# Kernel tuning notes

Hardware: AMD Instinct MI355X
Metric: run time of the kernel (lower is better)

The kernel has to match this reference:

```python
import jax, jax.numpy as jnp
import numpy as np

B, N, DIM = 1, 2048, 2048
H, KVH = 32, 4                 # query heads, kv heads
D = DIM // H                   # head_dim = 64
REP = H // KVH                 # queries per kv = 8
KV_DIM = D * KVH               # 256


def _rope_tables(n, d, base=10000.0):
    inv = 1.0 / (base ** (np.arange(0, d, 2, dtype=np.float32) / d))
    t = np.arange(n, dtype=np.float32)
    freqs = np.outer(t, inv)                      # [n, d/2]
    emb = np.concatenate([freqs, freqs], axis=-1)  # [n, d]
    return jnp.asarray(np.cos(emb)), jnp.asarray(np.sin(emb))


def setup_inputs() -> dict:
    key = jax.random.key(0)
    ks = jax.random.split(key, 5)
    s = 0.02
    cos, sin = _rope_tables(N, D)
    return {
        "x": jax.random.normal(ks[0], (B, N, DIM), jnp.float32),
        "Wq": jax.random.normal(ks[1], (DIM, DIM), jnp.float32) * s,
        "Wk": jax.random.normal(ks[2], (KV_DIM, DIM), jnp.float32) * s,
        "Wv": jax.random.normal(ks[3], (KV_DIM, DIM), jnp.float32) * s,
        "Wo": jax.random.normal(ks[4], (DIM, DIM), jnp.float32) * s,
        "cos": cos,
        "sin": sin,
    }


def _rotate_half(t):
    d2 = t.shape[-1] // 2
    return jnp.concatenate([-t[..., d2:], t[..., :d2]], axis=-1)


def reference(x, Wq, Wk, Wv, Wo, cos, sin):
    b, n, _ = x.shape
    # projections (nn.Linear: x @ W.T)
    q = (x @ Wq.T).reshape(b, n, H, D).transpose(0, 2, 1, 3)     # b h n d
    k = (x @ Wk.T).reshape(b, n, KVH, D).transpose(0, 2, 1, 3)   # b g n d
    v = (x @ Wv.T).reshape(b, n, KVH, D).transpose(0, 2, 1, 3)
    # RoPE
    c = cos[None, None, :, :]
    s = sin[None, None, :, :]
    q = q * c + _rotate_half(q) * s
    k = k * c + _rotate_half(k) * s
    # expand KV heads (repeat_interleave over head dim)
    k = jnp.repeat(k, REP, axis=1)   # b h n d
    v = jnp.repeat(v, REP, axis=1)
    # causal attention with materialized scores (faithful to source)
    scale = 1.0 / jnp.sqrt(jnp.asarray(D, x.dtype))
    scores = jnp.einsum('bhld,bhsd->bhls', q, k) * scale
    causal = jnp.tril(jnp.ones((n, n), bool))
    scores = jnp.where(causal[None, None], scores, jnp.asarray(-jnp.inf, x.dtype))
    attn = jax.nn.softmax(scores, axis=-1)
    y = jnp.einsum('bhls,bhsd->bhld', attn, v)       # b h n d
    y = y.transpose(0, 2, 1, 3).reshape(b, n, DIM)   # b n (h d)
    return y @ Wo.T
```

## Files before the change

kernel.cpp:

```cpp
#include <hip/hip_runtime.h>

typedef unsigned short u16;
typedef __attribute__((ext_vector_type(8))) short short8;
typedef __attribute__((ext_vector_type(4))) float floatx4;

#define N_TOK 2048
#define DIM   2048
#define NH    32
#define NKVH  4
#define HD    64
#define KVD   256

__device__ __forceinline__ float bf2f(u16 u) {
  union { unsigned i; float f; } c; c.i = ((unsigned)u) << 16; return c.f;
}
__device__ __forceinline__ u16 f2bf(float f) {
  union { float f; unsigned i; } c; c.f = f;
  unsigned x = c.i;
  return (u16)((x + 0x7fffu + ((x >> 16) & 1u)) >> 16);
}

__device__ __forceinline__ void gload16(const u16* g, u16* l) {
#if defined(__has_builtin) && __has_builtin(__builtin_amdgcn_global_load_lds)
  __builtin_amdgcn_global_load_lds(
      (const __attribute__((address_space(1))) void*)g,
      (__attribute__((address_space(3))) void*)l, 16, 0, 0);
#else
  *(short8*)l = *(const short8*)g;
#endif
}

#define C_X  1048576
#define C_WQ 2097152
#define C_WK 2228224
#define C_WV 2359296
#define C_WO 3407872
__global__ __launch_bounds__(256) void cvt_all(const float* __restrict__ x,
                                               const float* __restrict__ wq,
                                               const float* __restrict__ wk,
                                               const float* __restrict__ wv,
                                               const float* __restrict__ wo,
                                               u16* __restrict__ dst) {
  int i = blockIdx.x * 256 + threadIdx.x;
  const float* src; int off;
  if      (i < C_X)  { src = x;  off = 0; }
  else if (i < C_WQ) { src = wq; off = C_X; }
  else if (i < C_WK) { src = wk; off = C_WQ; }
  else if (i < C_WV) { src = wv; off = C_WK; }
  else               { src = wo; off = C_WV; }
  float4 v = ((const float4*)src)[i - off];
  ushort4 o;
  o.x = f2bf(v.x); o.y = f2bf(v.y); o.z = f2bf(v.z); o.w = f2bf(v.w);
  ((ushort4*)dst)[i] = o;
}


__global__ __launch_bounds__(256) void gemm_qkv(const u16* __restrict__ A,
                                                const u16* __restrict__ Wq,
                                                const u16* __restrict__ Wk,
                                                const u16* __restrict__ Wv,
                                                const float* __restrict__ cs,
                                                const float* __restrict__ sn,
                                                u16* __restrict__ Qp,
                                                u16* __restrict__ Kp,
                                                u16* __restrict__ Vp) {
  __shared__ __align__(16) u16 As[2][64 * 32];
  __shared__ __align__(16) u16 Bs[2][128 * 32];
  const int tid  = threadIdx.x;
  const int lane = tid & 63;
  const int w    = tid >> 6;
  const int r    = lane & 15, q = lane >> 4;
  const int tm = blockIdx.x & 31;
  const int tn = blockIdx.x >> 5;
  const int wm = w & 1, wn = w >> 1;
  const int K = DIM;

  const u16* W; int wrow0;
  if (tn < 16)      { W = Wq; wrow0 = tn * 128; }
  else if (tn < 18) { W = Wk; wrow0 = (tn - 16) * 128; }
  else              { W = Wv; wrow0 = (tn - 18) * 128; }

  const int srow   = tid >> 2;
  const int schunk = (tid & 3) ^ ((srow >> 1) & 3);
  const int scol   = schunk * 8;
  const u16* ga = A + (size_t)(tm * 64 + srow) * K + scol;
  const u16* gb = W + (size_t)(wrow0 + srow) * K + scol;

  const int rsw = (q ^ ((r >> 1) & 3)) * 8;

  floatx4 acc[2][4];
#pragma unroll
  for (int a = 0; a < 2; ++a)
#pragma unroll
    for (int b = 0; b < 4; ++b) acc[a][b] = (floatx4){0.f, 0.f, 0.f, 0.f};

  auto stage = [&](int b, int k0) {
    gload16(ga + k0, &As[b][tid * 8]);
    gload16(gb + k0, &Bs[b][tid * 8]);
    gload16(gb + k0 + (size_t)64 * K, &Bs[b][tid * 8 + 2048]);
  };

  stage(0, 0);
  __syncthreads();
  int cb = 0;
  for (int k0 = 0; k0 < K; k0 += 32) {
    if (k0 + 32 < K) stage(cb ^ 1, k0 + 32);

    short8 af[2], bf[4];
#pragma unroll
    for (int mi = 0; mi < 2; ++mi)
      af[mi] = *(const short8*)&As[cb][(wm * 32 + mi * 16 + r) * 32 + rsw];
#pragma unroll
    for (int nj = 0; nj < 4; ++nj)
      bf[nj] = *(const short8*)&Bs[cb][(wn * 64 + nj * 16 + r) * 32 + rsw];
#pragma unroll
    for (int mi = 0; mi < 2; ++mi)
#pragma unroll
      for (int nj = 0; nj < 4; ++nj)
        acc[mi][nj] = __builtin_amdgcn_mfma_f32_16x16x32_bf16(af[mi], bf[nj], acc[mi][nj], 0, 0, 0);

    __syncthreads();
    cb ^= 1;
  }

  if (tn < 18) {
    const int head = (tn < 16) ? (tn * 2 + wn) : ((tn - 16) * 2 + wn);
#pragma unroll
    for (int mi = 0; mi < 2; ++mi)
#pragma unroll
      for (int g = 0; g < 4; ++g) {
        int row = tm * 64 + wm * 32 + mi * 16 + 4 * q + g;
        const float* crow  = cs + (size_t)row * 64;
        const float* srow2 = sn + (size_t)row * 64;
#pragma unroll
        for (int nj = 0; nj < 2; ++nj) {
          int d = nj * 16 + r;
          float x0 = acc[mi][nj][g];
          float x1 = acc[mi][nj + 2][g];
          float o0 = x0 * crow[d]      - x1 * srow2[d];
          float o1 = x1 * crow[d + 32] + x0 * srow2[d + 32];
          int qq = d >> 3, j = d & 7;
          int lslot = (qq * 16 + (row & 15)) * 8 + j;
          if (tn < 16) {
            int sq = row >> 5, ii = (row >> 4) & 1;
            size_t base = ((size_t)(head * 64 + sq) * 4 + ii * 2) * 512 + lslot;
            Qp[base]       = f2bf(o0);
            Qp[base + 512] = f2bf(o1);
          } else {
            int kt = row >> 6, t = (row >> 4) & 3;
            size_t base = ((size_t)(head * 32 + kt) * 8 + t * 2) * 512 + lslot;
            Kp[base]       = f2bf(o0);
            Kp[base + 512] = f2bf(o1);
          }
        }
      }
  } else {
#pragma unroll
    for (int mi = 0; mi < 2; ++mi)
#pragma unroll
      for (int nj = 0; nj < 4; ++nj) {
        int col  = (tn - 18) * 128 + wn * 64 + nj * 16 + r;
        int kvh  = col >> 6;
        int t    = (col & 63) >> 4;
        int rr   = col & 15;
        int row0 = tm * 64 + wm * 32 + mi * 16 + 4 * q;
        int kt   = row0 >> 6;
        int wk   = row0 & 63;
        int s    = wk >> 5;
        int qq   = (wk & 31) >> 3;
        int j0   = wk & 7;
        uint2 pk;
        pk.x = (unsigned)f2bf(acc[mi][nj][0]) | ((unsigned)f2bf(acc[mi][nj][1]) << 16);
        pk.y = (unsigned)f2bf(acc[mi][nj][2]) | ((unsigned)f2bf(acc[mi][nj][3]) << 16);
        size_t idx = ((size_t)(kvh * 32 + kt) * 8 + s * 4 + t) * 512 + (qq * 16 + rr) * 8 + j0;
        *(uint2*)(Vp + idx) = pk;
      }
  }
}

__global__ __launch_bounds__(256) void gemm_out(const u16* __restrict__ A,
                                                const u16* __restrict__ W,
                                                float* __restrict__ C) {
  __shared__ __align__(16) u16 As[2][64 * 32];
  __shared__ __align__(16) u16 Bs[2][128 * 32];
  const int tid  = threadIdx.x;
  const int lane = tid & 63;
  const int w    = tid >> 6;
  const int r    = lane & 15, q = lane >> 4;
  const int tn = blockIdx.x & 15;
  const int tm = blockIdx.x >> 4;
  const int wm = w & 1, wn = w >> 1;
  const int K = DIM;

  const int srow   = tid >> 2;
  const int schunk = (tid & 3) ^ ((srow >> 1) & 3);
  const int scol   = schunk * 8;
  const u16* ga = A + (size_t)(tm * 64 + srow) * K + scol;
  const u16* gb = W + (size_t)(tn * 128 + srow) * K + scol;

  const int rsw = (q ^ ((r >> 1) & 3)) * 8;

  floatx4 acc[2][4];
#pragma unroll
  for (int a = 0; a < 2; ++a)
#pragma unroll
    for (int b = 0; b < 4; ++b) acc[a][b] = (floatx4){0.f, 0.f, 0.f, 0.f};

  auto stage = [&](int b, int k0) {
    gload16(ga + k0, &As[b][tid * 8]);
    gload16(gb + k0, &Bs[b][tid * 8]);
    gload16(gb + k0 + (size_t)64 * K, &Bs[b][tid * 8 + 2048]);
  };

  stage(0, 0);
  __syncthreads();
  int cb = 0;
  for (int k0 = 0; k0 < K; k0 += 32) {
    if (k0 + 32 < K) stage(cb ^ 1, k0 + 32);

    short8 af[2], bf[4];
#pragma unroll
    for (int mi = 0; mi < 2; ++mi)
      af[mi] = *(const short8*)&As[cb][(wm * 32 + mi * 16 + r) * 32 + rsw];
#pragma unroll
    for (int nj = 0; nj < 4; ++nj)
      bf[nj] = *(const short8*)&Bs[cb][(wn * 64 + nj * 16 + r) * 32 + rsw];
#pragma unroll
    for (int mi = 0; mi < 2; ++mi)
#pragma unroll
      for (int nj = 0; nj < 4; ++nj)
        acc[mi][nj] = __builtin_amdgcn_mfma_f32_16x16x32_bf16(af[mi], bf[nj], acc[mi][nj], 0, 0, 0);

    __syncthreads();
    cb ^= 1;
  }

#pragma unroll
  for (int mi = 0; mi < 2; ++mi)
#pragma unroll
    for (int g = 0; g < 4; ++g) {
      int row = tm * 64 + wm * 32 + mi * 16 + 4 * q + g;
#pragma unroll
      for (int nj = 0; nj < 4; ++nj)
        C[(size_t)row * DIM + tn * 128 + wn * 64 + nj * 16 + r] = acc[mi][nj][g];
    }
}

__global__ __launch_bounds__(128, 2) void attn_mfma(const u16* __restrict__ Qp,
                                                    const u16* __restrict__ Kp,
                                                    const u16* __restrict__ Vp,
                                                    u16* __restrict__ Yb) {
  __shared__ __align__(16) u16 Pl[2][32][72];
  __shared__ float OcA[32][66];
  __shared__ float OcB[32][66];
  __shared__ float LcA[2][64], LcB[2][64];
  const int tid  = threadIdx.x;
  const int lane = tid & 63;
  const int w    = tid >> 6;
  const int r    = lane & 15;
  const int q    = lane >> 4;
  const int p    = blockIdx.x;
  const int h    = blockIdx.y;
  const int kvh  = h >> 3;
  const int jA   = 63 - p;
  const int jB   = p;
  const int baseqA = jA * 32, baseqB = jB * 32;
  const int tA = (jA >> 1) + 1, tB = (jB >> 1) + 1;
  const int ktmaxA = tA - 1, ktmaxB = tB - 1;

  short8 qfA[2][2], qfB[2][2];
#pragma unroll
  for (int i = 0; i < 2; ++i)
#pragma unroll
    for (int c = 0; c < 2; ++c) {
      qfA[i][c] = *(const short8*)(Qp + ((size_t)(h * 64 + jA) * 4 + i * 2 + c) * 512 + lane * 8);
      qfB[i][c] = *(const short8*)(Qp + ((size_t)(h * 64 + jB) * 4 + i * 2 + c) * 512 + lane * 8);
    }

  floatx4 OA[2][4], OB[2][4];
  float lsumA[2], lsumB[2];
#pragma unroll
  for (int i = 0; i < 2; ++i) {
    lsumA[i] = 0.f; lsumB[i] = 0.f;
#pragma unroll
    for (int t = 0; t < 4; ++t) {
      OA[i][t] = (floatx4){0.f, 0.f, 0.f, 0.f};
      OB[i][t] = (floatx4){0.f, 0.f, 0.f, 0.f};
    }
  }

  const u16* Kbase = Kp + (size_t)(kvh * 32) * 8 * 512;
  const u16* Vbase = Vp + (size_t)(kvh * 32) * 8 * 512;

  auto loadK = [&](int kt, short8 (&kf)[4][2]) {
    const u16* kb = Kbase + (size_t)kt * 8 * 512 + lane * 8;
#pragma unroll
    for (int t = 0; t < 4; ++t) {
      kf[t][0] = *(const short8*)(kb + (t * 2 + 0) * 512);
      kf[t][1] = *(const short8*)(kb + (t * 2 + 1) * 512);
    }
  };

  auto body = [&](int kt, int ktmax, int baseq,
                  short8 (&qf)[2][2], floatx4 (&O)[2][4], float (&lsum)[2],
                  short8 (&kc)[4][2], short8 (&kn)[4][2]) {
    short8 vb[2][4];
    {
      const u16* vbp = Vbase + (size_t)kt * 8 * 512 + lane * 8;
#pragma unroll
      for (int s = 0; s < 2; ++s)
#pragma unroll
        for (int t = 0; t < 4; ++t)
          vb[s][t] = *(const short8*)(vbp + (s * 4 + t) * 512);
    }

    loadK(kt + 2 <= ktmax ? kt + 2 : ktmax, kn);

    floatx4 ST[2][4];
#pragma unroll
    for (int i = 0; i < 2; ++i)
#pragma unroll
      for (int t = 0; t < 4; ++t) ST[i][t] = (floatx4){0.f, 0.f, 0.f, 0.f};
#pragma unroll
    for (int t = 0; t < 4; ++t)
#pragma unroll
      for (int i = 0; i < 2; ++i) {
        ST[i][t] = __builtin_amdgcn_mfma_f32_16x16x32_bf16(kc[t][0], qf[i][0], ST[i][t], 0, 0, 0);
        ST[i][t] = __builtin_amdgcn_mfma_f32_16x16x32_bf16(kc[t][1], qf[i][1], ST[i][t], 0, 0, 0);
      }

    if (kt == ktmax) {
#pragma unroll
      for (int i = 0; i < 2; ++i) {
        int qrow = baseq + 16 * i + r;
#pragma unroll
        for (int t = 0; t < 4; ++t) {
          int key = kt * 64 + 16 * t + 4 * q;
#pragma unroll
          for (int g = 0; g < 4; ++g)
            if (key + g > qrow) ST[i][t][g] = -1e30f;
        }
      }
    }

#pragma unroll
    for (int i = 0; i < 2; ++i)
#pragma unroll
      for (int t = 0; t < 4; ++t) {
        float p0 = __expf(0.125f * ST[i][t][0]);
        float p1 = __expf(0.125f * ST[i][t][1]);
        float p2 = __expf(0.125f * ST[i][t][2]);
        float p3 = __expf(0.125f * ST[i][t][3]);
        lsum[i] += (p0 + p1) + (p2 + p3);
        uint2 pk;
        pk.x = (unsigned)f2bf(p0) | ((unsigned)f2bf(p1) << 16);
        pk.y = (unsigned)f2bf(p2) | ((unsigned)f2bf(p3) << 16);
        *(uint2*)&Pl[w][16 * i + r][16 * t + 4 * q] = pk;
      }

#pragma unroll
    for (int s = 0; s < 2; ++s)
#pragma unroll
      for (int i = 0; i < 2; ++i) {
        short8 pa = *(const short8*)&Pl[w][16 * i + r][32 * s + 8 * q];
#pragma unroll
        for (int t = 0; t < 4; ++t)
          O[i][t] = __builtin_amdgcn_mfma_f32_16x16x32_bf16(pa, vb[s][t], O[i][t], 0, 0, 0);
      }
  };

  auto runloop = [&](int start, int ktmax, int baseq,
                     short8 (&qf)[2][2], floatx4 (&O)[2][4], float (&lsum)[2]) {
    if (start > ktmax) return;
    short8 kA[4][2], kB[4][2];
    loadK(start, kA);
    for (int kt = start; kt <= ktmax; kt += 4) {
      body(kt, ktmax, baseq, qf, O, lsum, kA, kB);
      if (kt + 2 <= ktmax) body(kt + 2, ktmax, baseq, qf, O, lsum, kB, kA);
    }
  };

  runloop(w, ktmaxA, baseqA, qfA, OA, lsumA);
  const int sB = (w + tA) & 1;
  runloop(sB, ktmaxB, baseqB, qfB, OB, lsumB);

  if (w == 1) {
#pragma unroll
    for (int i = 0; i < 2; ++i) {
#pragma unroll
      for (int t = 0; t < 4; ++t)
#pragma unroll
        for (int g = 0; g < 4; ++g)
          OcA[(i * 4 + t) * 4 + g][lane] = OA[i][t][g];
      LcA[i][lane] = lsumA[i];
    }
  } else {
#pragma unroll
    for (int i = 0; i < 2; ++i) {
#pragma unroll
      for (int t = 0; t < 4; ++t)
#pragma unroll
        for (int g = 0; g < 4; ++g)
          OcB[(i * 4 + t) * 4 + g][lane] = OB[i][t][g];
      LcB[i][lane] = lsumB[i];
    }
  }
  __syncthreads();

  auto finalize = [&](int baseq, floatx4 (&O)[2][4], float (&lsum)[2]) {
#pragma unroll
    for (int i = 0; i < 2; ++i) {
      lsum[i] += __shfl_xor(lsum[i], 16);
      lsum[i] += __shfl_xor(lsum[i], 32);
    }
#pragma unroll
    for (int i = 0; i < 2; ++i) {
      float inv[4];
#pragma unroll
      for (int g = 0; g < 4; ++g)
        inv[g] = 1.f / __shfl(lsum[i], 4 * q + g);
#pragma unroll
      for (int g = 0; g < 4; ++g) {
        u16* yp = Yb + (size_t)(baseq + 16 * i + 4 * q + g) * DIM + h * 64 + r;
        yp[0]  = f2bf(O[i][0][g] * inv[g]);
        yp[16] = f2bf(O[i][1][g] * inv[g]);
        yp[32] = f2bf(O[i][2][g] * inv[g]);
        yp[48] = f2bf(O[i][3][g] * inv[g]);
      }
    }
  };

  if (w == 0) {
#pragma unroll
    for (int i = 0; i < 2; ++i) {
#pragma unroll
      for (int t = 0; t < 4; ++t)
#pragma unroll
        for (int g = 0; g < 4; ++g)
          OA[i][t][g] += OcA[(i * 4 + t) * 4 + g][lane];
      lsumA[i] += LcA[i][lane];
    }
    finalize(baseqA, OA, lsumA);
  } else {
#pragma unroll
    for (int i = 0; i < 2; ++i) {
#pragma unroll
      for (int t = 0; t < 4; ++t)
#pragma unroll
        for (int g = 0; g < 4; ++g)
          OB[i][t][g] += OcB[(i * 4 + t) * 4 + g][lane];
      lsumB[i] += LcB[i][lane];
    }
    finalize(baseqB, OB, lsumB);
  }
}

extern "C" void kernel_launch(void* const* d_in, const int* in_sizes, int n_in,
                              void* d_out, int out_size, void* d_ws, size_t ws_size,
                              hipStream_t stream) {
  const float* x  = (const float*)d_in[0];
  const float* Wq = (const float*)d_in[1];
  const float* Wk = (const float*)d_in[2];
  const float* Wv = (const float*)d_in[3];
  const float* Wo = (const float*)d_in[4];
  const float* cs = (const float*)d_in[5];
  const float* sn = (const float*)d_in[6];

  u16* ws  = (u16*)d_ws;
  u16* xb  = ws;
  u16* Wqb = xb  + (size_t)N_TOK * DIM;
  u16* Wkb = Wqb + (size_t)DIM * DIM;
  u16* Wvb = Wkb + (size_t)KVD * DIM;
  u16* Wob = Wvb + (size_t)KVD * DIM;
  u16* Qp  = Wob + (size_t)DIM * DIM;
  u16* Kp  = Qp  + (size_t)N_TOK * DIM;
  u16* Vp  = Kp  + (size_t)N_TOK * KVD;
  u16* Yb  = Vp  + (size_t)N_TOK * KVD;

  cvt_all<<<dim3(13312), 256, 0, stream>>>(x, Wq, Wk, Wv, Wo, ws);

  gemm_qkv<<<dim3(640), 256, 0, stream>>>(xb, Wqb, Wkb, Wvb, cs, sn, Qp, Kp, Vp);

  attn_mfma<<<dim3(32, 32), 128, 0, stream>>>(Qp, Kp, Vp, Yb);

  gemm_out<<<dim3(512), 256, 0, stream>>>(Yb, Wob, (float*)d_out);
}
```

Baseline: 208.4 us.

## Load A fragments directly to registers and store B in MFMA fragment order

Both projection GEMMs stop staging the A tile in LDS. Each wave now loads its A fragments straight from global memory into registers, prefetched one k-step ahead. The B tile is staged in LDS in MFMA-fragment order, so each lane reads a contiguous 16-byte slot without a swizzle. This cuts LDS traffic and footprint, but the A rows are now read redundantly by the two waves sharing wm, and the global A loads are strided 16-byte accesses per row.

New measurement: 282.1 us. 35.4% more time.

```diff
diff --git a/kernel.cpp b/kernel.cpp
--- a/kernel.cpp
+++ b/kernel.cpp
@@ -64,8 +64,7 @@
                                                 u16* __restrict__ Qp,
                                                 u16* __restrict__ Kp,
                                                 u16* __restrict__ Vp) {
-  __shared__ __align__(16) u16 As[2][64 * 32];
-  __shared__ __align__(16) u16 Bs[2][128 * 32];
+  __shared__ __align__(16) u16 Bs[2][8 * 512];
   const int tid  = threadIdx.x;
   const int lane = tid & 63;
   const int w    = tid >> 6;
@@ -80,13 +79,12 @@
   else if (tn < 18) { W = Wk; wrow0 = (tn - 16) * 128; }
   else              { W = Wv; wrow0 = (tn - 18) * 128; }
 
-  const int srow   = tid >> 2;
-  const int schunk = (tid & 3) ^ ((srow >> 1) & 3);
-  const int scol   = schunk * 8;
-  const u16* ga = A + (size_t)(tm * 64 + srow) * K + scol;
-  const u16* gb = W + (size_t)(wrow0 + srow) * K + scol;
-
-  const int rsw = (q ^ ((r >> 1) & 3)) * 8;
+  const int sr = tid & 15, sq8 = ((tid >> 4) & 3) * 8, sf = tid >> 6;
+  const u16* gb0 = W + (size_t)(wrow0 + sf * 16 + sr) * K + sq8;
+  const u16* gb1 = W + (size_t)(wrow0 + (sf + 4) * 16 + sr) * K + sq8;
+
+  const u16* ga0 = A + (size_t)(tm * 64 + wm * 32 + r) * K + q * 8;
+  const u16* ga1 = ga0 + (size_t)16 * K;
 
   floatx4 acc[2][4];
 #pragma unroll
@@ -94,32 +92,36 @@
 #pragma unroll
     for (int b = 0; b < 4; ++b) acc[a][b] = (floatx4){0.f, 0.f, 0.f, 0.f};
 
-  auto stage = [&](int b, int k0) {
-    gload16(ga + k0, &As[b][tid * 8]);
-    gload16(gb + k0, &Bs[b][tid * 8]);
-    gload16(gb + k0 + (size_t)64 * K, &Bs[b][tid * 8 + 2048]);
-  };
-
-  stage(0, 0);
+  auto stageB = [&](int b, int k0) {
+    gload16(gb0 + k0, &Bs[b][tid * 8]);
+    gload16(gb1 + k0, &Bs[b][2048 + tid * 8]);
+  };
+
+  short8 afc[2], afn[2];
+  stageB(0, 0);
+  afc[0] = *(const short8*)(ga0);
+  afc[1] = *(const short8*)(ga1);
   __syncthreads();
   int cb = 0;
   for (int k0 = 0; k0 < K; k0 += 32) {
-    if (k0 + 32 < K) stage(cb ^ 1, k0 + 32);
-
-    short8 af[2], bf[4];
+    if (k0 + 32 < K) {
+      stageB(cb ^ 1, k0 + 32);
+      afn[0] = *(const short8*)(ga0 + k0 + 32);
+      afn[1] = *(const short8*)(ga1 + k0 + 32);
+    }
+
+    short8 bf[4];
+#pragma unroll
+    for (int nj = 0; nj < 4; ++nj)
+      bf[nj] = *(const short8*)&Bs[cb][(wn * 4 + nj) * 512 + lane * 8];
 #pragma unroll
     for (int mi = 0; mi < 2; ++mi)
-      af[mi] = *(const short8*)&As[cb][(wm * 32 + mi * 16 + r) * 32 + rsw];
-#pragma unroll
-    for (int nj = 0; nj < 4; ++nj)
-      bf[nj] = *(const short8*)&Bs[cb][(wn * 64 + nj * 16 + r) * 32 + rsw];
-#pragma unroll
-    for (int mi = 0; mi < 2; ++mi)
 #pragma unroll
       for (int nj = 0; nj < 4; ++nj)
-        acc[mi][nj] = __builtin_amdgcn_mfma_f32_16x16x32_bf16(af[mi], bf[nj], acc[mi][nj], 0, 0, 0);
+        acc[mi][nj] = __builtin_amdgcn_mfma_f32_16x16x32_bf16(afc[mi], bf[nj], acc[mi][nj], 0, 0, 0);
 
     __syncthreads();
+    afc[0] = afn[0]; afc[1] = afn[1];
     cb ^= 1;
   }
 
@@ -181,8 +183,7 @@
 __global__ __launch_bounds__(256) void gemm_out(const u16* __restrict__ A,
                                                 const u16* __restrict__ W,
                                                 float* __restrict__ C) {
-  __shared__ __align__(16) u16 As[2][64 * 32];
-  __shared__ __align__(16) u16 Bs[2][128 * 32];
+  __shared__ __align__(16) u16 Bs[2][8 * 512];
   const int tid  = threadIdx.x;
   const int lane = tid & 63;
   const int w    = tid >> 6;
@@ -192,13 +193,12 @@
   const int wm = w & 1, wn = w >> 1;
   const int K = DIM;
 
-  const int srow   = tid >> 2;
-  const int schunk = (tid & 3) ^ ((srow >> 1) & 3);
-  const int scol   = schunk * 8;
-  const u16* ga = A + (size_t)(tm * 64 + srow) * K + scol;
-  const u16* gb = W + (size_t)(tn * 128 + srow) * K + scol;
-
-  const int rsw = (q ^ ((r >> 1) & 3)) * 8;
+  const int sr = tid & 15, sq8 = ((tid >> 4) & 3) * 8, sf = tid >> 6;
+  const u16* gb0 = W + (size_t)(tn * 128 + sf * 16 + sr) * K + sq8;
+  const u16* gb1 = W + (size_t)(tn * 128 + (sf + 4) * 16 + sr) * K + sq8;
+
+  const u16* ga0 = A + (size_t)(tm * 64 + wm * 32 + r) * K + q * 8;
+  const u16* ga1 = ga0 + (size_t)16 * K;
 
   floatx4 acc[2][4];
 #pragma unroll
@@ -206,32 +206,36 @@
 #pragma unroll
     for (int b = 0; b < 4; ++b) acc[a][b] = (floatx4){0.f, 0.f, 0.f, 0.f};
 
-  auto stage = [&](int b, int k0) {
-    gload16(ga + k0, &As[b][tid * 8]);
-    gload16(gb + k0, &Bs[b][tid * 8]);
-    gload16(gb + k0 + (size_t)64 * K, &Bs[b][tid * 8 + 2048]);
-  };
-
-  stage(0, 0);
+  auto stageB = [&](int b, int k0) {
+    gload16(gb0 + k0, &Bs[b][tid * 8]);
+    gload16(gb1 + k0, &Bs[b][2048 + tid * 8]);
+  };
+
+  short8 afc[2], afn[2];
+  stageB(0, 0);
+  afc[0] = *(const short8*)(ga0);
+  afc[1] = *(const short8*)(ga1);
   __syncthreads();
   int cb = 0;
   for (int k0 = 0; k0 < K; k0 += 32) {
-    if (k0 + 32 < K) stage(cb ^ 1, k0 + 32);
-
-    short8 af[2], bf[4];
+    if (k0 + 32 < K) {
+      stageB(cb ^ 1, k0 + 32);
+      afn[0] = *(const short8*)(ga0 + k0 + 32);
+      afn[1] = *(const short8*)(ga1 + k0 + 32);
+    }
+
+    short8 bf[4];
+#pragma unroll
+    for (int nj = 0; nj < 4; ++nj)
+      bf[nj] = *(const short8*)&Bs[cb][(wn * 4 + nj) * 512 + lane * 8];
 #pragma unroll
     for (int mi = 0; mi < 2; ++mi)
-      af[mi] = *(const short8*)&As[cb][(wm * 32 + mi * 16 + r) * 32 + rsw];
-#pragma unroll
-    for (int nj = 0; nj < 4; ++nj)
-      bf[nj] = *(const short8*)&Bs[cb][(wn * 64 + nj * 16 + r) * 32 + rsw];
-#pragma unroll
-    for (int mi = 0; mi < 2; ++mi)
 #pragma unroll
       for (int nj = 0; nj < 4; ++nj)
-        acc[mi][nj] = __builtin_amdgcn_mfma_f32_16x16x32_bf16(af[mi], bf[nj], acc[mi][nj], 0, 0, 0);
+        acc[mi][nj] = __builtin_amdgcn_mfma_f32_16x16x32_bf16(afc[mi], bf[nj], acc[mi][nj], 0, 0, 0);
 
     __syncthreads();
+    afc[0] = afn[0]; afc[1] = afn[1];
     cb ^= 1;
   }
 
```

## Triple-buffer GEMM K-loop with explicit vmcnt waits and fragment-ordered LDS layout

Applied to the files above, without the earlier changes.

Both the QKV and output projection GEMMs move from double to triple buffering, keeping three global-to-LDS stages in flight. Explicit s_waitcnt vmcnt counts and raw s_barrier replace the blanket __syncthreads, so later loads stay outstanding while MFMAs run. The LDS staging layout changes to MFMA fragment order, so each lane reads 16 contiguous bytes and the XOR swizzle is dropped. LDS use grows by half, and the hand-written wait counts depend on the exact number of loads per stage.

Measured after the change: 250.4 us. +20.2%, slower.

```diff
diff --git a/kernel.cpp b/kernel.cpp
--- a/kernel.cpp
+++ b/kernel.cpp
@@ -64,8 +64,8 @@
                                                 u16* __restrict__ Qp,
                                                 u16* __restrict__ Kp,
                                                 u16* __restrict__ Vp) {
-  __shared__ __align__(16) u16 As[2][64 * 32];
-  __shared__ __align__(16) u16 Bs[2][128 * 32];
+  __shared__ __align__(16) u16 As[3][2048];
+  __shared__ __align__(16) u16 Bs[3][4096];
   const int tid  = threadIdx.x;
   const int lane = tid & 63;
   const int w    = tid >> 6;
@@ -80,13 +80,10 @@
   else if (tn < 18) { W = Wk; wrow0 = (tn - 16) * 128; }
   else              { W = Wv; wrow0 = (tn - 18) * 128; }
 
-  const int srow   = tid >> 2;
-  const int schunk = (tid & 3) ^ ((srow >> 1) & 3);
-  const int scol   = schunk * 8;
-  const u16* ga = A + (size_t)(tm * 64 + srow) * K + scol;
-  const u16* gb = W + (size_t)(wrow0 + srow) * K + scol;
-
-  const int rsw = (q ^ ((r >> 1) & 3)) * 8;
+  const int sr = tid & 15, sc8 = ((tid >> 4) & 3) * 8, sf = tid >> 6;
+  const u16* gaS = A + (size_t)(tm * 64 + sf * 16 + sr) * K + sc8;
+  const u16* gb0 = W + (size_t)(wrow0 + sf * 16 + sr) * K + sc8;
+  const u16* gb1 = W + (size_t)(wrow0 + (sf + 4) * 16 + sr) * K + sc8;
 
   floatx4 acc[2][4];
 #pragma unroll
@@ -95,32 +92,39 @@
     for (int b = 0; b < 4; ++b) acc[a][b] = (floatx4){0.f, 0.f, 0.f, 0.f};
 
   auto stage = [&](int b, int k0) {
-    gload16(ga + k0, &As[b][tid * 8]);
-    gload16(gb + k0, &Bs[b][tid * 8]);
-    gload16(gb + k0 + (size_t)64 * K, &Bs[b][tid * 8 + 2048]);
+    gload16(gaS + k0, &As[b][tid * 8]);
+    gload16(gb0 + k0, &Bs[b][tid * 8]);
+    gload16(gb1 + k0, &Bs[b][2048 + tid * 8]);
   };
 
   stage(0, 0);
-  __syncthreads();
+  stage(1, 32);
+  stage(2, 64);
   int cb = 0;
-  for (int k0 = 0; k0 < K; k0 += 32) {
-    if (k0 + 32 < K) stage(cb ^ 1, k0 + 32);
+  for (int kt = 0; kt < 64; ++kt) {
+    if (kt < 62)       asm volatile("s_waitcnt vmcnt(6)" ::: "memory");
+    else if (kt == 62) asm volatile("s_waitcnt vmcnt(3)" ::: "memory");
+    else               asm volatile("s_waitcnt vmcnt(0)" ::: "memory");
+    __builtin_amdgcn_s_barrier();
+    __builtin_amdgcn_sched_barrier(0);
 
     short8 af[2], bf[4];
 #pragma unroll
     for (int mi = 0; mi < 2; ++mi)
-      af[mi] = *(const short8*)&As[cb][(wm * 32 + mi * 16 + r) * 32 + rsw];
+      af[mi] = *(const short8*)&As[cb][(wm * 2 + mi) * 512 + lane * 8];
 #pragma unroll
     for (int nj = 0; nj < 4; ++nj)
-      bf[nj] = *(const short8*)&Bs[cb][(wn * 64 + nj * 16 + r) * 32 + rsw];
+      bf[nj] = *(const short8*)&Bs[cb][(wn * 4 + nj) * 512 + lane * 8];
 #pragma unroll
     for (int mi = 0; mi < 2; ++mi)
 #pragma unroll
       for (int nj = 0; nj < 4; ++nj)
         acc[mi][nj] = __builtin_amdgcn_mfma_f32_16x16x32_bf16(af[mi], bf[nj], acc[mi][nj], 0, 0, 0);
 
-    __syncthreads();
-    cb ^= 1;
+    __builtin_amdgcn_sched_barrier(0);
+    __builtin_amdgcn_s_barrier();
+    if (kt + 3 < 64) stage(cb, (kt + 3) * 32);
+    cb = (cb == 2) ? 0 : cb + 1;
   }
 
   if (tn < 18) {
@@ -147,8 +151,8 @@
             Qp[base]       = f2bf(o0);
             Qp[base + 512] = f2bf(o1);
           } else {
-            int kt = row >> 6, t = (row >> 4) & 3;
-            size_t base = ((size_t)(head * 32 + kt) * 8 + t * 2) * 512 + lslot;
+            int kt2 = row >> 6, t = (row >> 4) & 3;
+            size_t base = ((size_t)(head * 32 + kt2) * 8 + t * 2) * 512 + lslot;
             Kp[base]       = f2bf(o0);
             Kp[base + 512] = f2bf(o1);
           }
@@ -164,7 +168,7 @@
         int t    = (col & 63) >> 4;
         int rr   = col & 15;
         int row0 = tm * 64 + wm * 32 + mi * 16 + 4 * q;
-        int kt   = row0 >> 6;
+        int kt2  = row0 >> 6;
         int wk   = row0 & 63;
         int s    = wk >> 5;
         int qq   = (wk & 31) >> 3;
@@ -172,7 +176,7 @@
         uint2 pk;
         pk.x = (unsigned)f2bf(acc[mi][nj][0]) | ((unsigned)f2bf(acc[mi][nj][1]) << 16);
         pk.y = (unsigned)f2bf(acc[mi][nj][2]) | ((unsigned)f2bf(acc[mi][nj][3]) << 16);
-        size_t idx = ((size_t)(kvh * 32 + kt) * 8 + s * 4 + t) * 512 + (qq * 16 + rr) * 8 + j0;
+        size_t idx = ((size_t)(kvh * 32 + kt2) * 8 + s * 4 + t) * 512 + (qq * 16 + rr) * 8 + j0;
         *(uint2*)(Vp + idx) = pk;
       }
   }
@@ -181,8 +185,8 @@
 __global__ __launch_bounds__(256) void gemm_out(const u16* __restrict__ A,
                                                 const u16* __restrict__ W,
                                                 float* __restrict__ C) {
-  __shared__ __align__(16) u16 As[2][64 * 32];
-  __shared__ __align__(16) u16 Bs[2][128 * 32];
+  __shared__ __align__(16) u16 As[3][2048];
+  __shared__ __align__(16) u16 Bs[3][4096];
   const int tid  = threadIdx.x;
   const int lane = tid & 63;
   const int w    = tid >> 6;
@@ -192,13 +196,10 @@
   const int wm = w & 1, wn = w >> 1;
   const int K = DIM;
 
-  const int srow   = tid >> 2;
-  const int schunk = (tid & 3) ^ ((srow >> 1) & 3);
-  const int scol   = schunk * 8;
-  const u16* ga = A + (size_t)(tm * 64 + srow) * K + scol;
-  const u16* gb = W + (size_t)(tn * 128 + srow) * K + scol;
-
-  const int rsw = (q ^ ((r >> 1) & 3)) * 8;
+  const int sr = tid & 15, sc8 = ((tid >> 4) & 3) * 8, sf = tid >> 6;
+  const u16* gaS = A + (size_t)(tm * 64 + sf * 16 + sr) * K + sc8;
+  const u16* gb0 = W + (size_t)(tn * 128 + sf * 16 + sr) * K + sc8;
+  const u16* gb1 = W + (size_t)(tn * 128 + (sf + 4) * 16 + sr) * K + sc8;
 
   floatx4 acc[2][4];
 #pragma unroll
@@ -207,32 +208,39 @@
     for (int b = 0; b < 4; ++b) acc[a][b] = (floatx4){0.f, 0.f, 0.f, 0.f};
 
   auto stage = [&](int b, int k0) {
-    gload16(ga + k0, &As[b][tid * 8]);
-    gload16(gb + k0, &Bs[b][tid * 8]);
-    gload16(gb + k0 + (size_t)64 * K, &Bs[b][tid * 8 + 2048]);
+    gload16(gaS + k0, &As[b][tid * 8]);
+    gload16(gb0 + k0, &Bs[b][tid * 8]);
+    gload16(gb1 + k0, &Bs[b][2048 + tid * 8]);
   };
 
   stage(0, 0);
-  __syncthreads();
+  stage(1, 32);
+  stage(2, 64);
   int cb = 0;
-  for (int k0 = 0; k0 < K; k0 += 32) {
-    if (k0 + 32 < K) stage(cb ^ 1, k0 + 32);
+  for (int kt = 0; kt < 64; ++kt) {
+    if (kt < 62)       asm volatile("s_waitcnt vmcnt(6)" ::: "memory");
+    else if (kt == 62) asm volatile("s_waitcnt vmcnt(3)" ::: "memory");
+    else               asm volatile("s_waitcnt vmcnt(0)" ::: "memory");
+    __builtin_amdgcn_s_barrier();
+    __builtin_amdgcn_sched_barrier(0);
 
     short8 af[2], bf[4];
 #pragma unroll
     for (int mi = 0; mi < 2; ++mi)
-      af[mi] = *(const short8*)&As[cb][(wm * 32 + mi * 16 + r) * 32 + rsw];
+      af[mi] = *(const short8*)&As[cb][(wm * 2 + mi) * 512 + lane * 8];
 #pragma unroll
     for (int nj = 0; nj < 4; ++nj)
-      bf[nj] = *(const short8*)&Bs[cb][(wn * 64 + nj * 16 + r) * 32 + rsw];
+      bf[nj] = *(const short8*)&Bs[cb][(wn * 4 + nj) * 512 + lane * 8];
 #pragma unroll
     for (int mi = 0; mi < 2; ++mi)
 #pragma unroll
       for (int nj = 0; nj < 4; ++nj)
         acc[mi][nj] = __builtin_amdgcn_mfma_f32_16x16x32_bf16(af[mi], bf[nj], acc[mi][nj], 0, 0, 0);
 
-    __syncthreads();
-    cb ^= 1;
+    __builtin_amdgcn_sched_barrier(0);
+    __builtin_amdgcn_s_barrier();
+    if (kt + 3 < 64) stage(cb, (kt + 3) * 32);
+    cb = (cb == 2) ? 0 : cb + 1;
   }
 
 #pragma unroll
```
